# Kernel tuning notes

Measured on AMD Instinct MI355X. Metric: run time of the kernel, lower is better.

Reference implementation:

```python
import jax, jax.numpy as jnp
import numpy as np

N_NODES = 100000
N_EDGES = 3200000
D = 64
NUM_RELS = 20
HID_ATTR = 32
OUT_ATTR = 10


def setup_inputs() -> dict:
    key = jax.random.key(0)
    ks = jax.random.split(key, 10)
    h = jax.random.normal(ks[0], (N_NODES, D), dtype=jnp.float32)
    src = jax.random.randint(ks[1], (N_EDGES,), 0, N_NODES)
    dst = jax.random.randint(ks[2], (N_EDGES,), 0, N_NODES)
    etype = jax.random.randint(ks[3], (N_EDGES,), 0, NUM_RELS)
    # RGCN relation weights (num_bases == num_rels, so no basis decomposition)
    s1 = (2.0 / (D + D)) ** 0.5 * (2.0 ** 0.5)  # xavier w/ relu gain, approx
    W1 = jax.random.normal(ks[4], (NUM_RELS, D, D), dtype=jnp.float32) * s1
    W2 = jax.random.normal(ks[5], (NUM_RELS, D, D), dtype=jnp.float32) * s1
    # Attributor MLP params (torch Linear: y = x @ W.T + b; stored here as [in,out])
    A1_w = jax.random.normal(ks[6], (D, HID_ATTR), dtype=jnp.float32) * (1.0 / D ** 0.5)
    A1_b = jnp.zeros((HID_ATTR,), dtype=jnp.float32)
    A2_w = jax.random.normal(ks[7], (HID_ATTR, OUT_ATTR), dtype=jnp.float32) * (1.0 / HID_ATTR ** 0.5)
    A2_b = jnp.zeros((OUT_ATTR,), dtype=jnp.float32)
    return {"h": h, "src": src, "dst": dst, "etype": etype,
            "W1": W1, "W2": W2, "A1_w": A1_w, "A1_b": A1_b,
            "A2_w": A2_w, "A2_b": A2_b}


def _rgcn_layer(h, W, src, dst, etype, activation):
    # Transform all nodes by every relation once (avoids [E,d,d] weight gather),
    # then gather the relation-specific transformed source feature per edge.
    n = h.shape[0]
    t = jnp.einsum('nd,rdo->rno', h, W)          # [R, N, d_out]
    msg = t[etype, src]                           # [E, d_out] irregular gather
    agg = jax.ops.segment_sum(msg, dst, num_segments=n)  # scatter-sum to nodes
    return activation(agg) if activation is not None else agg


def reference(h, src, dst, etype, W1, W2, A1_w, A1_b, A2_w, A2_b):
    # hidden RGCN layer (relu), output RGCN layer (no activation, no bias)
    h1 = _rgcn_layer(h, W1, src, dst, etype, jax.nn.relu)
    h2 = _rgcn_layer(h1, W2, src, dst, etype, None)
    # mean_nodes over the single graph -> [1, D]; Attributor MLP (dropout in eval = identity)
    g = jnp.mean(h2, axis=0, keepdims=True)
    a = jax.nn.relu(g @ A1_w + A1_b)
    a = jax.nn.sigmoid(a @ A2_w + A2_b)
    return (h2, a)
```

## Files before the change

### kernel.cpp

```cpp
#include <hip/hip_runtime.h>
#include <hip/hip_bf16.h>
#include <math.h>
#include <stdint.h>

#define N_NODES 100000
#define N_EDGES 3200000
#define D 64
#define NUM_RELS 20
#define HID_ATTR 32
#define OUT_ATTR 10
#define PADR 72

#define BUCKET_DSTS 256
#define NB 391
#define PA_THREADS 512
#define PA_EPT 16
#define PA_CHUNK (PA_THREADS * PA_EPT)
#define PA_GRID 391
#define PB_BINS (BUCKET_DSTS * NUM_RELS)

typedef __attribute__((ext_vector_type(8))) short bf16x8;
typedef __attribute__((ext_vector_type(4))) float f32x4;

static __device__ __forceinline__ unsigned short f2bf(float x) {
    unsigned u = __builtin_bit_cast(unsigned, x);
    unsigned r = (u + 0x7FFFu + ((u >> 16) & 1u)) >> 16;
    return (unsigned short)r;
}
static __device__ __forceinline__ float bf2f(unsigned short b) {
    return __builtin_bit_cast(float, (unsigned)b << 16);
}
static __device__ __forceinline__ float bf2f_lo(unsigned u) {
    return __builtin_bit_cast(float, u << 16);
}
static __device__ __forceinline__ float bf2f_hi(unsigned u) {
    return __builtin_bit_cast(float, u & 0xFFFF0000u);
}
static __device__ __forceinline__ unsigned cvt_pk_bf16(float lo, float hi) {
    unsigned r;
    asm("v_cvt_pk_bf16_f32 %0, %1, %2" : "=v"(r) : "v"(lo), "v"(hi));
    return r;
}


__global__ void hist_bucket_kernel(const int* __restrict__ dst, int* __restrict__ hist) {
    __shared__ int h[NB];
    for (int i = threadIdx.x; i < NB; i += PA_THREADS) h[i] = 0;
    __syncthreads();
    int base = blockIdx.x * PA_CHUNK;
#pragma unroll
    for (int k = 0; k < PA_EPT; ++k) {
        int e = base + k * PA_THREADS + threadIdx.x;
        if (e < N_EDGES) atomicAdd(&h[dst[e] >> 8], 1);
    }
    __syncthreads();
    for (int i = threadIdx.x; i < NB; i += PA_THREADS)
        if (h[i]) atomicAdd(&hist[i], h[i]);
}

__global__ void scan_bucket_kernel(const int* __restrict__ hist, int* __restrict__ bbase,
                                   int* __restrict__ bcur, int* __restrict__ off_node) {
    __shared__ int s[512];
    int t = threadIdx.x;
    int v = (t < NB) ? hist[t] : 0;
    s[t] = v;
    __syncthreads();
    for (int d2 = 1; d2 < 512; d2 <<= 1) {
        int x = (t >= d2) ? s[t - d2] : 0;
        __syncthreads();
        s[t] += x;
        __syncthreads();
    }
    if (t < NB) {
        int b = s[t] - v;
        bbase[t] = b;
        bcur[t] = b;
    }
    if (t == 0) {
        bbase[NB] = N_EDGES;
        off_node[N_NODES] = N_EDGES;
    }
}

__global__ __launch_bounds__(PA_THREADS) void passA_kernel(
    const int* __restrict__ src, const int* __restrict__ dst,
    const int* __restrict__ etype, int* __restrict__ bcur,
    unsigned* __restrict__ tmp) {
    __shared__ int h[NB];
    __shared__ int gb[NB];
    __shared__ int c[NB];
    for (int i = threadIdx.x; i < NB; i += PA_THREADS) h[i] = 0;
    __syncthreads();
    int base = blockIdx.x * PA_CHUNK;
    int d[PA_EPT];
#pragma unroll
    for (int k = 0; k < PA_EPT; ++k) {
        int e = base + k * PA_THREADS + threadIdx.x;
        d[k] = (e < N_EDGES) ? dst[e] : -1;
        if (d[k] >= 0) atomicAdd(&h[d[k] >> 8], 1);
    }
    __syncthreads();
    for (int i = threadIdx.x; i < NB; i += PA_THREADS) {
        int n = h[i];
        gb[i] = n ? atomicAdd(&bcur[i], n) : 0;
        c[i] = 0;
    }
    __syncthreads();
#pragma unroll
    for (int k = 0; k < PA_EPT; ++k) {
        int e = base + k * PA_THREADS + threadIdx.x;
        if (d[k] >= 0) {
            int b = d[k] >> 8;
            int sv = src[e], r = etype[e];
            int pos = gb[b] + atomicAdd(&c[b], 1);
            tmp[pos] = ((unsigned)(d[k] & 255) << 22) | ((unsigned)sv << 5) | (unsigned)r;
        }
    }
}

__global__ __launch_bounds__(512) void passB_kernel(
    const unsigned* __restrict__ tmp, const int* __restrict__ bbase,
    int* __restrict__ edgedata, int* __restrict__ off_node) {
    __shared__ int binpos[PB_BINS];
    __shared__ int ssum[512];
    int t = threadIdx.x;
    int b = blockIdx.x;
    int beg = bbase[b], end = bbase[b + 1];
    for (int i = t; i < PB_BINS; i += 512) binpos[i] = 0;
    __syncthreads();
    for (int i = beg + t; i < end; i += 512) {
        unsigned v = tmp[i];
        int key = (int)(v >> 22) * NUM_RELS + (int)(v & 31u);
        atomicAdd(&binpos[key], 1);
    }
    __syncthreads();
    int loc[10];
    int sum = 0;
#pragma unroll
    for (int j = 0; j < 10; ++j) {
        loc[j] = sum;
        sum += binpos[t * 10 + j];
    }
    ssum[t] = sum;
    __syncthreads();
    for (int d2 = 1; d2 < 512; d2 <<= 1) {
        int x = (t >= d2) ? ssum[t - d2] : 0;
        __syncthreads();
        ssum[t] += x;
        __syncthreads();
    }
    int tbase = beg + ((t > 0) ? ssum[t - 1] : 0);
#pragma unroll
    for (int j = 0; j < 10; ++j) binpos[t * 10 + j] = tbase + loc[j];
    __syncthreads();
    for (int dl = t; dl < BUCKET_DSTS; dl += 512)
        off_node[b * BUCKET_DSTS + dl] = binpos[dl * NUM_RELS];
    __syncthreads();
    for (int i = beg + t; i < end; i += 512) {
        unsigned v = tmp[i];
        int key = (int)(v >> 22) * NUM_RELS + (int)(v & 31u);
        int pos = atomicAdd(&binpos[key], 1);
        edgedata[pos] = (int)(((v >> 5) & 0x1FFFFu) | ((v & 31u) << 17));
    }
}


__global__ void f2b_kernel(const float* __restrict__ in, unsigned short* __restrict__ out,
                           int n4) {
    int i = blockIdx.x * 256 + threadIdx.x;
    if (i >= n4) return;
    float4 v = ((const float4*)in)[i];
    ushort4 o;
    o.x = f2bf(v.x); o.y = f2bf(v.y); o.z = f2bf(v.z); o.w = f2bf(v.w);
    ((ushort4*)out)[i] = o;
}

__global__ void wconv_kernel(const float* __restrict__ W, unsigned short* __restrict__ Wb) {
    int r = blockIdx.x;
    for (int i = threadIdx.x; i < D * D; i += 256) {
        int d2 = i >> 6, o = i & 63;
        Wb[(size_t)r * (D * D) + o * D + d2] = f2bf(W[(size_t)r * (D * D) + d2 * D + o]);
    }
}

__global__ __launch_bounds__(256, 3) void fused_layer(
    const unsigned short* __restrict__ xb, const unsigned short* __restrict__ Wb,
    const int* __restrict__ edgedata, const int* __restrict__ off_node,
    unsigned short* __restrict__ xbout, float* __restrict__ h2out, int mode) {
    __shared__ __align__(16) unsigned short A[NUM_RELS * 16 * PADR];
    int wave = threadIdx.x >> 6, lane = threadIdx.x & 63;
    int grp = lane >> 4, l4 = lane & 15;
    int m = wave * 4 + grp;
    int colb = l4 * 4;

    for (int i = threadIdx.x; i < NUM_RELS * 16 * PADR / 8; i += 256)
        ((int4*)A)[i] = (int4){0, 0, 0, 0};
    __syncthreads();

    int n0 = blockIdx.x * 16;
    int beg = off_node[n0 + m];
    int end = off_node[n0 + m + 1];
    int cnt = end - beg;
    int nf = cnt >> 3, tl = cnt & 7;
    int nfmax = max(nf, __shfl_xor(nf, 16));
    nfmax = max(nfmax, __shfl_xor(nfmax, 32));
    int tlmax = max(tl, __shfl_xor(tl, 16));
    tlmax = max(tlmax, __shfl_xor(tlmax, 32));

    float a0 = 0.f, a1 = 0.f, a2 = 0.f, a3 = 0.f;
    int qcur = -1;
    unsigned short* Am = A + (unsigned)m * PADR + (unsigned)colb;

    int i = beg;
    int ew[8];
    if (nf > 0) {
#pragma unroll
        for (int j = 0; j < 8; ++j) ew[j] = edgedata[i + j];
    }
    for (int g = 0; g < nfmax; ++g) {
        bool act = g < nf;
        if (act) {
            int ewc[8];
#pragma unroll
            for (int j = 0; j < 8; ++j) ewc[j] = ew[j];
            if (g + 1 < nf) {
#pragma unroll
                for (int j = 0; j < 8; ++j) ew[j] = edgedata[i + 8 + j];
            }
            uint2 xv[8];
#pragma unroll
            for (int j = 0; j < 8; ++j)
                xv[j] = *(const uint2*)(xb + (((unsigned)(ewc[j] & 0x1FFFF)) << 6)
                                        + (unsigned)colb);
#pragma unroll
            for (int j = 0; j < 8; ++j) {
                int q = ewc[j] >> 17;
                bool keep = (q == qcur);
                a0 = (keep ? a0 : 0.f) + bf2f_lo(xv[j].x);
                a1 = (keep ? a1 : 0.f) + bf2f_hi(xv[j].x);
                a2 = (keep ? a2 : 0.f) + bf2f_lo(xv[j].y);
                a3 = (keep ? a3 : 0.f) + bf2f_hi(xv[j].y);
                uint2 o;
                o.x = cvt_pk_bf16(a0, a1);
                o.y = cvt_pk_bf16(a2, a3);
                *(uint2*)(Am + (unsigned)q * (16 * PADR)) = o;
                qcur = q;
            }
            i += 8;
        }
    }
    for (int k = 0; k < tlmax; ++k) {
        if (k < tl) {
            int ewc = edgedata[i + k];
            uint2 v = *(const uint2*)(xb + (((unsigned)(ewc & 0x1FFFF)) << 6)
                                      + (unsigned)colb);
            int q = ewc >> 17;
            bool keep = (q == qcur);
            a0 = (keep ? a0 : 0.f) + bf2f_lo(v.x);
            a1 = (keep ? a1 : 0.f) + bf2f_hi(v.x);
            a2 = (keep ? a2 : 0.f) + bf2f_lo(v.y);
            a3 = (keep ? a3 : 0.f) + bf2f_hi(v.y);
            uint2 o;
            o.x = cvt_pk_bf16(a0, a1);
            o.y = cvt_pk_bf16(a2, a3);
            *(uint2*)(Am + (unsigned)q * (16 * PADR)) = o;
            qcur = q;
        }
    }
    __syncthreads();

    {
        int lrow = lane & 15, lhi = lane >> 4;
        f32x4 C = {0.f, 0.f, 0.f, 0.f};
        for (int q = 0; q < NUM_RELS; ++q) {
            const unsigned short* Arow = &A[(q * 16 + lrow) * PADR + lhi * 8];
            bf16x8 aa0 = *(const bf16x8*)(Arow);
            bf16x8 aa1 = *(const bf16x8*)(Arow + 32);
            const unsigned short* wrow = Wb + ((size_t)q << 12)
                                         + (size_t)(wave * 16 + lrow) * D + lhi * 8;
            bf16x8 b0 = *(const bf16x8*)(wrow);
            bf16x8 b1 = *(const bf16x8*)(wrow + 32);
            C = __builtin_amdgcn_mfma_f32_16x16x32_bf16(aa0, b0, C, 0, 0, 0);
            C = __builtin_amdgcn_mfma_f32_16x16x32_bf16(aa1, b1, C, 0, 0, 0);
        }
#pragma unroll
        for (int reg = 0; reg < 4; ++reg) {
            int node = n0 + lhi * 4 + reg;
            int col = wave * 16 + lrow;
            if (mode == 1)
                xbout[(size_t)node * D + col] = f2bf(fmaxf(C[reg], 0.f));
            else
                h2out[(size_t)node * D + col] = C[reg];
        }
    }
}


__global__ void colsum_kernel(const float* __restrict__ h2,
                              float* __restrict__ g, int n) {
    __shared__ float s[256];
    int tid = threadIdx.x;
    int col = tid & 63;
    int rowgrp = (blockIdx.x * blockDim.x + tid) >> 6;
    int nrowgrp = (gridDim.x * blockDim.x) >> 6;
    float acc = 0.0f;
    for (int row = rowgrp; row < n; row += nrowgrp)
        acc += h2[(size_t)row * D + col];
    s[tid] = acc;
    __syncthreads();
    if (tid < 64) {
        acc = s[tid] + s[tid + 64] + s[tid + 128] + s[tid + 192];
        atomicAdd(&g[col], acc);
    }
}

__global__ void mlp_kernel(const float* __restrict__ g,
                           const float* __restrict__ A1w,
                           const float* __restrict__ A1b,
                           const float* __restrict__ A2w,
                           const float* __restrict__ A2b,
                           float* __restrict__ out, float invN) {
    __shared__ float a1[HID_ATTR];
    int t = threadIdx.x;
    if (t < HID_ATTR) {
        float acc = A1b[t];
#pragma unroll
        for (int d2 = 0; d2 < D; ++d2)
            acc = fmaf(g[d2] * invN, A1w[d2 * HID_ATTR + t], acc);
        a1[t] = fmaxf(acc, 0.0f);
    }
    __syncthreads();
    if (t < OUT_ATTR) {
        float acc = A2b[t];
#pragma unroll
        for (int j = 0; j < HID_ATTR; ++j)
            acc = fmaf(a1[j], A2w[j * OUT_ATTR + t], acc);
        out[t] = 1.0f / (1.0f + expf(-acc));
    }
}


extern "C" void kernel_launch(void* const* d_in, const int* in_sizes, int n_in,
                              void* d_out, int out_size, void* d_ws, size_t ws_size,
                              hipStream_t stream) {
    const float* h   = (const float*)d_in[0];
    const int* src   = (const int*)d_in[1];
    const int* dst   = (const int*)d_in[2];
    const int* etype = (const int*)d_in[3];
    const float* W1  = (const float*)d_in[4];
    const float* W2  = (const float*)d_in[5];
    const float* A1w = (const float*)d_in[6];
    const float* A1b = (const float*)d_in[7];
    const float* A2w = (const float*)d_in[8];
    const float* A2b = (const float*)d_in[9];

    float* out_h2 = (float*)d_out;
    float* out_a  = out_h2 + (size_t)N_NODES * D;

    int* base       = (int*)d_ws;
    float* gsum     = (float*)base;
    int* hist_b     = base + 64;
    int* bbase      = base + 456;
    int* bcur       = base + 848;
    int* off_node   = base + 1240;
    unsigned* tmp   = (unsigned*)(base + 101592);
    int* edgedata   = base + 3301592;
    unsigned short* xb  = (unsigned short*)(base + 6501592);
    unsigned short* xb2 = (unsigned short*)(base + 9701592);
    unsigned short* w1b = (unsigned short*)(base + 12901592);
    unsigned short* w2b = (unsigned short*)(base + 12942552);

    hipMemsetAsync(hist_b, 0, NB * sizeof(int), stream);
    hipMemsetAsync(gsum, 0, 64 * sizeof(float), stream);

    hist_bucket_kernel<<<PA_GRID, PA_THREADS, 0, stream>>>(dst, hist_b);
    scan_bucket_kernel<<<1, 512, 0, stream>>>(hist_b, bbase, bcur, off_node);
    passA_kernel<<<PA_GRID, PA_THREADS, 0, stream>>>(src, dst, etype, bcur, tmp);
    passB_kernel<<<NB, 512, 0, stream>>>(tmp, bbase, edgedata, off_node);

    wconv_kernel<<<NUM_RELS, 256, 0, stream>>>(W1, w1b);
    wconv_kernel<<<NUM_RELS, 256, 0, stream>>>(W2, w2b);
    f2b_kernel<<<(N_NODES * D / 4 + 255) / 256, 256, 0, stream>>>(h, xb, N_NODES * D / 4);

    fused_layer<<<N_NODES / 16, 256, 0, stream>>>(xb, w1b, edgedata, off_node,
                                                  xb2, nullptr, 1);
    fused_layer<<<N_NODES / 16, 256, 0, stream>>>(xb2, w2b, edgedata, off_node,
                                                  nullptr, out_h2, 2);

    colsum_kernel<<<512, 256, 0, stream>>>(out_h2, gsum, N_NODES);
    mlp_kernel<<<1, 64, 0, stream>>>(gsum, A1w, A1b, A2w, A2b,
                                     out_a, 1.0f / (float)N_NODES);
}
```

Measured before the change: 666.0 us.

## Split each node's edge gather across two half-groups by relation range

Each destination node's edges, already sorted by relation, are split at relation 10 into two halves, each handled by its own 16-lane group. Blocks become 512 threads so twice as many lanes gather features in parallel, and the extra half-offsets are written during the sort pass. Because the halves cover disjoint relations, they write separate slices of the shared aggregation buffer without conflict. Only the first four waves run the MFMA transform, so the added waves sit idle in that phase, and occupancy depends on the larger block fitting the register and LDS budget.

After: 643.0 us. -3.4%, faster.

```diff
diff --git a/kernel.cpp b/kernel.cpp
--- a/kernel.cpp
+++ b/kernel.cpp
@@ -18,6 +18,7 @@
 #define PA_CHUNK (PA_THREADS * PA_EPT)
 #define PA_GRID 391
 #define PB_BINS (BUCKET_DSTS * NUM_RELS)
+#define REL_HALF 10
 
 typedef __attribute__((ext_vector_type(8))) short bf16x8;
 typedef __attribute__((ext_vector_type(4))) float f32x4;
@@ -120,7 +121,8 @@
 
 __global__ __launch_bounds__(512) void passB_kernel(
     const unsigned* __restrict__ tmp, const int* __restrict__ bbase,
-    int* __restrict__ edgedata, int* __restrict__ off_node) {
+    int* __restrict__ edgedata, int* __restrict__ off_node,
+    int* __restrict__ off_half) {
     __shared__ int binpos[PB_BINS];
     __shared__ int ssum[512];
     int t = threadIdx.x;
@@ -153,8 +155,10 @@
 #pragma unroll
     for (int j = 0; j < 10; ++j) binpos[t * 10 + j] = tbase + loc[j];
     __syncthreads();
-    for (int dl = t; dl < BUCKET_DSTS; dl += 512)
+    for (int dl = t; dl < BUCKET_DSTS; dl += 512) {
         off_node[b * BUCKET_DSTS + dl] = binpos[dl * NUM_RELS];
+        off_half[b * BUCKET_DSTS + dl] = binpos[dl * NUM_RELS + REL_HALF];
+    }
     __syncthreads();
     for (int i = beg + t; i < end; i += 512) {
         unsigned v = tmp[i];
@@ -183,23 +187,27 @@
     }
 }
 
-__global__ __launch_bounds__(256, 3) void fused_layer(
+__global__ __launch_bounds__(512, 6) void fused_layer(
     const unsigned short* __restrict__ xb, const unsigned short* __restrict__ Wb,
     const int* __restrict__ edgedata, const int* __restrict__ off_node,
+    const int* __restrict__ off_half,
     unsigned short* __restrict__ xbout, float* __restrict__ h2out, int mode) {
     __shared__ __align__(16) unsigned short A[NUM_RELS * 16 * PADR];
     int wave = threadIdx.x >> 6, lane = threadIdx.x & 63;
     int grp = lane >> 4, l4 = lane & 15;
-    int m = wave * 4 + grp;
+    int gidx = wave * 4 + grp;
+    int m = gidx & 15;
+    int h = gidx >> 4;
     int colb = l4 * 4;
 
-    for (int i = threadIdx.x; i < NUM_RELS * 16 * PADR / 8; i += 256)
+    for (int i = threadIdx.x; i < NUM_RELS * 16 * PADR / 8; i += 512)
         ((int4*)A)[i] = (int4){0, 0, 0, 0};
     __syncthreads();
 
     int n0 = blockIdx.x * 16;
-    int beg = off_node[n0 + m];
-    int end = off_node[n0 + m + 1];
+    int node = n0 + m;
+    int beg = h ? off_half[node] : off_node[node];
+    int end = h ? off_node[node + 1] : off_half[node];
     int cnt = end - beg;
     int nf = cnt >> 3, tl = cnt & 7;
     int nfmax = max(nf, __shfl_xor(nf, 16));
@@ -269,7 +277,7 @@
     }
     __syncthreads();
 
-    {
+    if (wave < 4) {
         int lrow = lane & 15, lhi = lane >> 4;
         f32x4 C = {0.f, 0.f, 0.f, 0.f};
         for (int q = 0; q < NUM_RELS; ++q) {
@@ -285,12 +293,12 @@
         }
 #pragma unroll
         for (int reg = 0; reg < 4; ++reg) {
-            int node = n0 + lhi * 4 + reg;
+            int onode = n0 + lhi * 4 + reg;
             int col = wave * 16 + lrow;
             if (mode == 1)
-                xbout[(size_t)node * D + col] = f2bf(fmaxf(C[reg], 0.f));
+                xbout[(size_t)onode * D + col] = f2bf(fmaxf(C[reg], 0.f));
             else
-                h2out[(size_t)node * D + col] = C[reg];
+                h2out[(size_t)onode * D + col] = C[reg];
         }
     }
 }
@@ -363,12 +371,13 @@
     int* bbase      = base + 456;
     int* bcur       = base + 848;
     int* off_node   = base + 1240;
-    unsigned* tmp   = (unsigned*)(base + 101592);
-    int* edgedata   = base + 3301592;
-    unsigned short* xb  = (unsigned short*)(base + 6501592);
-    unsigned short* xb2 = (unsigned short*)(base + 9701592);
-    unsigned short* w1b = (unsigned short*)(base + 12901592);
-    unsigned short* w2b = (unsigned short*)(base + 12942552);
+    int* off_half   = base + 101592;
+    unsigned* tmp   = (unsigned*)(base + 201944);
+    int* edgedata   = base + 3401944;
+    unsigned short* xb  = (unsigned short*)(base + 6601944);
+    unsigned short* xb2 = (unsigned short*)(base + 9801944);
+    unsigned short* w1b = (unsigned short*)(base + 13001944);
+    unsigned short* w2b = (unsigned short*)(base + 13042904);
 
     hipMemsetAsync(hist_b, 0, NB * sizeof(int), stream);
     hipMemsetAsync(gsum, 0, 64 * sizeof(float), stream);
@@ -376,16 +385,16 @@
     hist_bucket_kernel<<<PA_GRID, PA_THREADS, 0, stream>>>(dst, hist_b);
     scan_bucket_kernel<<<1, 512, 0, stream>>>(hist_b, bbase, bcur, off_node);
     passA_kernel<<<PA_GRID, PA_THREADS, 0, stream>>>(src, dst, etype, bcur, tmp);
-    passB_kernel<<<NB, 512, 0, stream>>>(tmp, bbase, edgedata, off_node);
+    passB_kernel<<<NB, 512, 0, stream>>>(tmp, bbase, edgedata, off_node, off_half);
 
     wconv_kernel<<<NUM_RELS, 256, 0, stream>>>(W1, w1b);
     wconv_kernel<<<NUM_RELS, 256, 0, stream>>>(W2, w2b);
     f2b_kernel<<<(N_NODES * D / 4 + 255) / 256, 256, 0, stream>>>(h, xb, N_NODES * D / 4);
 
-    fused_layer<<<N_NODES / 16, 256, 0, stream>>>(xb, w1b, edgedata, off_node,
-                                                  xb2, nullptr, 1);
-    fused_layer<<<N_NODES / 16, 256, 0, stream>>>(xb2, w2b, edgedata, off_node,
-                                                  nullptr, out_h2, 2);
+    fused_layer<<<N_NODES / 16, 512, 0, stream>>>(xb, w1b, edgedata, off_node,
+                                                  off_half, xb2, nullptr, 1);
+    fused_layer<<<N_NODES / 16, 512, 0, stream>>>(xb2, w2b, edgedata, off_node,
+                                                  off_half, nullptr, out_h2, 2);
 
     colsum_kernel<<<512, 256, 0, stream>>>(out_h2, gsum, N_NODES);
     mlp_kernel<<<1, 64, 0, stream>>>(gsum, A1w, A1b, A2w, A2b,
```
